# Optimization experiments

Hardware: AMD Instinct MI355X
Metric: run time of the kernel (lower is better)

## Reference

```python
import jax, jax.numpy as jnp
import numpy as np

INPUT_SIZE = 64
HIDDEN = 128
NUM_CLASSES = 4
BATCH = 512
SEQ = 1024


def setup_inputs() -> dict:
    key = jax.random.key(0)
    ks = jax.random.split(key, 11)
    s_in = 1.0 / np.sqrt(INPUT_SIZE)
    s_h = 1.0 / np.sqrt(HIDDEN)
    inp = {
        "x": jax.random.normal(ks[0], (BATCH, SEQ, INPUT_SIZE), dtype=jnp.float32),
        # layer1: x_proj (4H, in), h_proj (4H, H), each with bias
        "Wx1": jax.random.uniform(ks[1], (4 * HIDDEN, INPUT_SIZE), minval=-s_in, maxval=s_in),
        "bx1": jax.random.uniform(ks[2], (4 * HIDDEN,), minval=-s_in, maxval=s_in),
        "Wh1": jax.random.uniform(ks[3], (4 * HIDDEN, HIDDEN), minval=-s_h, maxval=s_h),
        "bh1": jax.random.uniform(ks[4], (4 * HIDDEN,), minval=-s_h, maxval=s_h),
        # layer2: x_proj (4H, H), h_proj (4H, H)
        "Wx2": jax.random.uniform(ks[5], (4 * HIDDEN, HIDDEN), minval=-s_h, maxval=s_h),
        "bx2": jax.random.uniform(ks[6], (4 * HIDDEN,), minval=-s_h, maxval=s_h),
        "Wh2": jax.random.uniform(ks[7], (4 * HIDDEN, HIDDEN), minval=-s_h, maxval=s_h),
        "bh2": jax.random.uniform(ks[8], (4 * HIDDEN,), minval=-s_h, maxval=s_h),
        # classifier head (num_classes, H)
        "Wc": jax.random.uniform(ks[9], (NUM_CLASSES, HIDDEN), minval=-s_h, maxval=s_h),
        "bc": jax.random.uniform(ks[10], (NUM_CLASSES,), minval=-s_h, maxval=s_h),
    }
    return inp


def _cell(gates, c_prev):
    # torch Linear gate order after chunk(4): i, f, g, o
    i, f, g, o = jnp.split(gates, 4, axis=-1)
    c = jax.nn.sigmoid(f) * c_prev + jax.nn.sigmoid(i) * jnp.tanh(g)
    h = jax.nn.sigmoid(o) * jnp.tanh(c)
    return h, c


def reference(x, Wx1, bx1, Wh1, bh1, Wx2, bx2, Wh2, bh2, Wc, bc):
    B = x.shape[0]
    H = Wh1.shape[1]
    # Precompute input projections for all timesteps in one big GEMM: (B,S,4H)
    xg1 = jnp.einsum("bsi,gi->bsg", x, Wx1) + bx1 + bh1  # fold both biases
    xg1_t = jnp.swapaxes(xg1, 0, 1)  # (S, B, 4H) for scan

    def step(carry, xg_t):
        h1, c1, h2, c2 = carry
        gates1 = xg_t + h1 @ Wh1.T
        h1, c1 = _cell(gates1, c1)
        gates2 = h1 @ Wx2.T + bx2 + h2 @ Wh2.T + bh2
        h2, c2 = _cell(gates2, c2)
        return (h1, c1, h2, c2), None

    z = jnp.zeros((B, H), dtype=x.dtype)
    (h1, c1, h2, c2), _ = jax.lax.scan(step, (z, z, z, z), xg1_t)
    logits = h2 @ Wc.T + bc  # (B, num_classes)
    return logits
```

## Files before the change

kernel.cpp:

```cpp
#include <hip/hip_runtime.h>
#include <hip/hip_fp16.h>

namespace {

constexpr int kS = 1024;
constexpr int kI = 64;
constexpr int kH = 128;

typedef _Float16 f16x8 __attribute__((ext_vector_type(8)));
typedef float    f32x4 __attribute__((ext_vector_type(4)));

#define MFMA16(a, b, c) __builtin_amdgcn_mfma_f32_16x16x32_f16((a), (b), (c), 0, 0, 0)

__device__ __forceinline__ float rcpf(float x) {
#if __has_builtin(__builtin_amdgcn_rcpf)
  return __builtin_amdgcn_rcpf(x);
#else
  return 1.0f / x;
#endif
}
__device__ __forceinline__ float sigf(float x)  { return rcpf(1.0f + __expf(-x)); }
__device__ __forceinline__ float tanhff(float x){ return 1.0f - 2.0f * rcpf(1.0f + __expf(2.0f * x)); }

__device__ __forceinline__ f16x8 afrag(const float* __restrict__ W, int row,
                                       int k0, int ld) {
  const float4* p = reinterpret_cast<const float4*>(W + (size_t)row * ld + k0);
  const float4 u = p[0], v = p[1];
  f16x8 a;
  a[0] = (_Float16)u.x; a[1] = (_Float16)u.y; a[2] = (_Float16)u.z; a[3] = (_Float16)u.w;
  a[4] = (_Float16)v.x; a[5] = (_Float16)v.y; a[6] = (_Float16)v.z; a[7] = (_Float16)v.w;
  return a;
}

__global__ __launch_bounds__(1024) void lstm_l1(
    const float* __restrict__ x, const float* __restrict__ Wx1,
    const float* __restrict__ bx1, const float* __restrict__ Wh1,
    const float* __restrict__ bh1, _Float16* __restrict__ h1out)
{
  const int tid  = threadIdx.x;
  const int b0   = blockIdx.x * 2;
  const int w    = tid >> 6;
  const int q    = (tid >> 4) & 3;
  const int n    = tid & 15;
  const bool real = (n < 2);

  __shared__ __align__(16) _Float16 xB[8][8][2][8];
  __shared__ __align__(16) _Float16 hB[2][16][2][8];
  __shared__ __align__(16) float    zslot[4];
  __shared__ float gbuf[2][512];

  f16x8 A[2][6];
  {
    const int rb = w * 32 + (tid & 15);
#pragma unroll
    for (int s = 0; s < 2; ++s) {
      const int row = rb + s * 16;
      A[s][0] = afrag(Wx1, row, q * 8,       kI);
      A[s][1] = afrag(Wx1, row, 32 + q * 8,  kI);
#pragma unroll
      for (int kt = 0; kt < 4; ++kt)
        A[s][2 + kt] = afrag(Wh1, row, kt * 32 + q * 8, kH);
    }
  }

  float bI = 0.f, bF = 0.f, bG = 0.f, bO = 0.f, cst = 0.f;
  if (tid < 256) {
    const int j = tid & 127;
    bI = bx1[j]       + bh1[j];
    bF = bx1[j + 128] + bh1[j + 128];
    bG = bx1[j + 256] + bh1[j + 256];
    bO = bx1[j + 384] + bh1[j + 384];
  }
  if (tid < 256)      reinterpret_cast<_Float16*>(hB)[tid] = (_Float16)0.f;
  else if (tid < 260) zslot[tid - 256] = 0.f;

  const int   off = q * 32 + n * 16;
  const char* zp  = reinterpret_cast<const char*>(zslot);

  for (int t0 = 0; t0 < kS; t0 += 8) {
    {
      const int st = tid >> 7, sn = (tid >> 6) & 1, sk = tid & 63;
      const float v = x[((size_t)(b0 + sn) * kS + (size_t)(t0 + st)) * kI + sk];
      xB[st][sk >> 3][sn][sk & 7] = (_Float16)v;
    }
    __syncthreads();

    for (int dt = 0; dt < 8; ++dt) {
      const int t = t0 + dt;
      const char* xb = reinterpret_cast<const char*>(&xB[dt][0][0][0]);
      const char* hb = reinterpret_cast<const char*>(&hB[t & 1][0][0][0]);
      const f16x8 bf0 = *reinterpret_cast<const f16x8*>(real ? xb + off       : zp);
      const f16x8 bf1 = *reinterpret_cast<const f16x8*>(real ? xb + 128 + off : zp);
      const f16x8 bf2 = *reinterpret_cast<const f16x8*>(real ? hb + off       : zp);
      const f16x8 bf3 = *reinterpret_cast<const f16x8*>(real ? hb + 128 + off : zp);
      const f16x8 bf4 = *reinterpret_cast<const f16x8*>(real ? hb + 256 + off : zp);
      const f16x8 bf5 = *reinterpret_cast<const f16x8*>(real ? hb + 384 + off : zp);

      f32x4 d0 = {0.f, 0.f, 0.f, 0.f}, d1 = {0.f, 0.f, 0.f, 0.f};
      d0 = MFMA16(A[0][0], bf0, d0);  d1 = MFMA16(A[1][0], bf0, d1);
      d0 = MFMA16(A[0][1], bf1, d0);  d1 = MFMA16(A[1][1], bf1, d1);
      d0 = MFMA16(A[0][2], bf2, d0);  d1 = MFMA16(A[1][2], bf2, d1);
      d0 = MFMA16(A[0][3], bf3, d0);  d1 = MFMA16(A[1][3], bf3, d1);
      d0 = MFMA16(A[0][4], bf4, d0);  d1 = MFMA16(A[1][4], bf4, d1);
      d0 = MFMA16(A[0][5], bf5, d0);  d1 = MFMA16(A[1][5], bf5, d1);

      if (real) {
        *reinterpret_cast<f32x4*>(&gbuf[n][w * 32 + q * 4])      = d0;
        *reinterpret_cast<f32x4*>(&gbuf[n][w * 32 + 16 + q * 4]) = d1;
      }
      __syncthreads();

      if (tid < 256) {
        const int cc = tid >> 7, j = tid & 127;
        const float gi = gbuf[cc][j]       + bI;
        const float gf = gbuf[cc][j + 128] + bF;
        const float gg = gbuf[cc][j + 256] + bG;
        const float go = gbuf[cc][j + 384] + bO;
        cst = sigf(gf) * cst + sigf(gi) * tanhff(gg);
        const float h = sigf(go) * tanhff(cst);
        hB[(t + 1) & 1][j >> 3][cc][j & 7] = (_Float16)h;
        h1out[((size_t)(b0 + cc) * kS + (size_t)t) * kH + j] = (_Float16)h;
      }
      __syncthreads();
    }
  }
}

__global__ __launch_bounds__(1024) void lstm_l2(
    const _Float16* __restrict__ h1in,
    const float* __restrict__ Wx2, const float* __restrict__ bx2,
    const float* __restrict__ Wh2, const float* __restrict__ bh2,
    const float* __restrict__ Wc,  const float* __restrict__ bc,
    float* __restrict__ out)
{
  const int tid  = threadIdx.x;
  const int b0   = blockIdx.x * 2;
  const int w    = tid >> 6;
  const int q    = (tid >> 4) & 3;
  const int n    = tid & 15;
  const bool real = (n < 2);

  __shared__ __align__(16) _Float16 h1B[8][16][2][8];
  __shared__ __align__(16) _Float16 h2B[2][16][2][8];
  __shared__ __align__(16) float    zslot[4];
  __shared__ float gbuf[2][512];
  __shared__ float hfin[2][128];

  f16x8 A[2][8];
  {
    const int rb = w * 32 + (tid & 15);
#pragma unroll
    for (int s = 0; s < 2; ++s) {
      const int row = rb + s * 16;
#pragma unroll
      for (int kt = 0; kt < 4; ++kt) {
        A[s][kt]     = afrag(Wx2, row, kt * 32 + q * 8, kH);
        A[s][4 + kt] = afrag(Wh2, row, kt * 32 + q * 8, kH);
      }
    }
  }

  float bI = 0.f, bF = 0.f, bG = 0.f, bO = 0.f, cst = 0.f;
  if (tid < 256) {
    const int j = tid & 127;
    bI = bx2[j]       + bh2[j];
    bF = bx2[j + 128] + bh2[j + 128];
    bG = bx2[j + 256] + bh2[j + 256];
    bO = bx2[j + 384] + bh2[j + 384];
  }
  if (tid < 256)      reinterpret_cast<_Float16*>(h2B)[tid] = (_Float16)0.f;
  else if (tid < 260) zslot[tid - 256] = 0.f;

  const int   off = q * 32 + n * 16;
  const char* zp  = reinterpret_cast<const char*>(zslot);

  for (int t0 = 0; t0 < kS; t0 += 8) {
    {
#pragma unroll
      for (int e = tid; e < 2048; e += 1024) {
        const int st = e >> 8, sn = (e >> 7) & 1, sk = e & 127;
        h1B[st][sk >> 3][sn][sk & 7] =
            h1in[((size_t)(b0 + sn) * kS + (size_t)(t0 + st)) * kH + sk];
      }
    }
    __syncthreads();

    for (int dt = 0; dt < 8; ++dt) {
      const int t = t0 + dt;
      const char* xb = reinterpret_cast<const char*>(&h1B[dt][0][0][0]);
      const char* hb = reinterpret_cast<const char*>(&h2B[t & 1][0][0][0]);

      f32x4 d0 = {0.f, 0.f, 0.f, 0.f}, d1 = {0.f, 0.f, 0.f, 0.f};
      {
        const f16x8 bf0 = *reinterpret_cast<const f16x8*>(real ? xb + off       : zp);
        const f16x8 bf1 = *reinterpret_cast<const f16x8*>(real ? xb + 128 + off : zp);
        const f16x8 bf2 = *reinterpret_cast<const f16x8*>(real ? xb + 256 + off : zp);
        const f16x8 bf3 = *reinterpret_cast<const f16x8*>(real ? xb + 384 + off : zp);
        d0 = MFMA16(A[0][0], bf0, d0);  d1 = MFMA16(A[1][0], bf0, d1);
        d0 = MFMA16(A[0][1], bf1, d0);  d1 = MFMA16(A[1][1], bf1, d1);
        d0 = MFMA16(A[0][2], bf2, d0);  d1 = MFMA16(A[1][2], bf2, d1);
        d0 = MFMA16(A[0][3], bf3, d0);  d1 = MFMA16(A[1][3], bf3, d1);
      }
#if __has_builtin(__builtin_amdgcn_sched_barrier)
      __builtin_amdgcn_sched_barrier(0);
#endif
      {
        const f16x8 bf4 = *reinterpret_cast<const f16x8*>(real ? hb + off       : zp);
        const f16x8 bf5 = *reinterpret_cast<const f16x8*>(real ? hb + 128 + off : zp);
        const f16x8 bf6 = *reinterpret_cast<const f16x8*>(real ? hb + 256 + off : zp);
        const f16x8 bf7 = *reinterpret_cast<const f16x8*>(real ? hb + 384 + off : zp);
        d0 = MFMA16(A[0][4], bf4, d0);  d1 = MFMA16(A[1][4], bf4, d1);
        d0 = MFMA16(A[0][5], bf5, d0);  d1 = MFMA16(A[1][5], bf5, d1);
        d0 = MFMA16(A[0][6], bf6, d0);  d1 = MFMA16(A[1][6], bf6, d1);
        d0 = MFMA16(A[0][7], bf7, d0);  d1 = MFMA16(A[1][7], bf7, d1);
      }

      if (real) {
        *reinterpret_cast<f32x4*>(&gbuf[n][w * 32 + q * 4])      = d0;
        *reinterpret_cast<f32x4*>(&gbuf[n][w * 32 + 16 + q * 4]) = d1;
      }
      __syncthreads();

      if (tid < 256) {
        const int cc = tid >> 7, j = tid & 127;
        const float gi = gbuf[cc][j]       + bI;
        const float gf = gbuf[cc][j + 128] + bF;
        const float gg = gbuf[cc][j + 256] + bG;
        const float go = gbuf[cc][j + 384] + bO;
        cst = sigf(gf) * cst + sigf(gi) * tanhff(gg);
        const float h = sigf(go) * tanhff(cst);
        h2B[(t + 1) & 1][j >> 3][cc][j & 7] = (_Float16)h;
        if (t == kS - 1) hfin[cc][j] = h;
      }
      __syncthreads();
    }
  }

  if (tid < 8) {
    const int m = tid & 3, c = tid >> 2;
    const float* wr = Wc + (size_t)m * kH;
    float s0 = 0.f, s1 = 0.f, s2 = 0.f, s3 = 0.f;
#pragma unroll
    for (int j = 0; j < kH; j += 4) {
      s0 = fmaf(wr[j],     hfin[c][j],     s0);
      s1 = fmaf(wr[j + 1], hfin[c][j + 1], s1);
      s2 = fmaf(wr[j + 2], hfin[c][j + 2], s2);
      s3 = fmaf(wr[j + 3], hfin[c][j + 3], s3);
    }
    out[(size_t)(b0 + c) * 4 + m] = bc[m] + ((s0 + s1) + (s2 + s3));
  }
}

}

extern "C" void kernel_launch(void* const* d_in, const int* in_sizes, int n_in,
                              void* d_out, int out_size, void* d_ws, size_t ws_size,
                              hipStream_t stream) {
  const float* x   = (const float*)d_in[0];
  const float* Wx1 = (const float*)d_in[1];
  const float* bx1 = (const float*)d_in[2];
  const float* Wh1 = (const float*)d_in[3];
  const float* bh1 = (const float*)d_in[4];
  const float* Wx2 = (const float*)d_in[5];
  const float* bx2 = (const float*)d_in[6];
  const float* Wh2 = (const float*)d_in[7];
  const float* bh2 = (const float*)d_in[8];
  const float* Wc  = (const float*)d_in[9];
  const float* bc  = (const float*)d_in[10];

  _Float16* h1 = (_Float16*)d_ws;

  hipLaunchKernelGGL(lstm_l1, dim3(256), dim3(1024), 0, stream,
                     x, Wx1, bx1, Wh1, bh1, h1);
  hipLaunchKernelGGL(lstm_l2, dim3(256), dim3(1024), 0, stream,
                     h1, Wx2, bx2, Wh2, bh2, Wc, bc, (float*)d_out);
}
```

Measured before the change: 1.858 ms.

## Process one batch element per block and raise MFMA wave priority

Each workgroup now handles a single sequence instead of two, which doubles the grid so more independent recurrences run concurrently across CUs. The MFMA B-operand layout is simplified so only one column is real and the zero-slot indirection is removed. The MFMA sections are wrapped in s_setprio to favour the latency-critical matrix work. This relies on two 1024-thread blocks co-residing per CU; otherwise the doubled grid would serialize.

```diff
diff --git a/kernel.cpp b/kernel.cpp
--- a/kernel.cpp
+++ b/kernel.cpp
@@ -21,6 +21,13 @@
 }
 __device__ __forceinline__ float sigf(float x)  { return rcpf(1.0f + __expf(-x)); }
 __device__ __forceinline__ float tanhff(float x){ return 1.0f - 2.0f * rcpf(1.0f + __expf(2.0f * x)); }
+
+template <int P>
+__device__ __forceinline__ void prio() {
+#if __has_builtin(__builtin_amdgcn_s_setprio)
+  __builtin_amdgcn_s_setprio(P);
+#endif
+}
 
 __device__ __forceinline__ f16x8 afrag(const float* __restrict__ W, int row,
                                        int k0, int ld) {
@@ -37,17 +44,16 @@
     const float* __restrict__ bx1, const float* __restrict__ Wh1,
     const float* __restrict__ bh1, _Float16* __restrict__ h1out)
 {
-  const int tid  = threadIdx.x;
-  const int b0   = blockIdx.x * 2;
-  const int w    = tid >> 6;
-  const int q    = (tid >> 4) & 3;
-  const int n    = tid & 15;
-  const bool real = (n < 2);
-
-  __shared__ __align__(16) _Float16 xB[8][8][2][8];
-  __shared__ __align__(16) _Float16 hB[2][16][2][8];
-  __shared__ __align__(16) float    zslot[4];
-  __shared__ float gbuf[2][512];
+  const int tid = threadIdx.x;
+  const int b   = blockIdx.x;
+  const int w   = tid >> 6;
+  const int q   = (tid >> 4) & 3;
+  const int n   = tid & 15;
+  const bool real = (n == 0);
+
+  __shared__ __align__(16) _Float16 xB[8][8][8];
+  __shared__ __align__(16) _Float16 hB[2][16][8];
+  __shared__ float gbuf[512];
 
   f16x8 A[2][6];
   {
@@ -55,8 +61,8 @@
 #pragma unroll
     for (int s = 0; s < 2; ++s) {
       const int row = rb + s * 16;
-      A[s][0] = afrag(Wx1, row, q * 8,       kI);
-      A[s][1] = afrag(Wx1, row, 32 + q * 8,  kI);
+      A[s][0] = afrag(Wx1, row, q * 8,      kI);
+      A[s][1] = afrag(Wx1, row, 32 + q * 8, kI);
 #pragma unroll
       for (int kt = 0; kt < 4; ++kt)
         A[s][2 + kt] = afrag(Wh1, row, kt * 32 + q * 8, kH);
@@ -64,62 +70,60 @@
   }
 
   float bI = 0.f, bF = 0.f, bG = 0.f, bO = 0.f, cst = 0.f;
-  if (tid < 256) {
-    const int j = tid & 127;
-    bI = bx1[j]       + bh1[j];
-    bF = bx1[j + 128] + bh1[j + 128];
-    bG = bx1[j + 256] + bh1[j + 256];
-    bO = bx1[j + 384] + bh1[j + 384];
-  }
-  if (tid < 256)      reinterpret_cast<_Float16*>(hB)[tid] = (_Float16)0.f;
-  else if (tid < 260) zslot[tid - 256] = 0.f;
-
-  const int   off = q * 32 + n * 16;
-  const char* zp  = reinterpret_cast<const char*>(zslot);
+  if (tid < 128) {
+    bI = bx1[tid]       + bh1[tid];
+    bF = bx1[tid + 128] + bh1[tid + 128];
+    bG = bx1[tid + 256] + bh1[tid + 256];
+    bO = bx1[tid + 384] + bh1[tid + 384];
+    reinterpret_cast<_Float16*>(hB)[tid] = (_Float16)0.f;
+  }
+
+  const int boff = real ? (q * 16) : 0;
 
   for (int t0 = 0; t0 < kS; t0 += 8) {
-    {
-      const int st = tid >> 7, sn = (tid >> 6) & 1, sk = tid & 63;
-      const float v = x[((size_t)(b0 + sn) * kS + (size_t)(t0 + st)) * kI + sk];
-      xB[st][sk >> 3][sn][sk & 7] = (_Float16)v;
+    if (tid < 512) {
+      const int st = tid >> 6, sk = tid & 63;
+      xB[st][sk >> 3][sk & 7] =
+          (_Float16)x[((size_t)b * kS + (size_t)(t0 + st)) * kI + sk];
     }
     __syncthreads();
 
     for (int dt = 0; dt < 8; ++dt) {
       const int t = t0 + dt;
-      const char* xb = reinterpret_cast<const char*>(&xB[dt][0][0][0]);
-      const char* hb = reinterpret_cast<const char*>(&hB[t & 1][0][0][0]);
-      const f16x8 bf0 = *reinterpret_cast<const f16x8*>(real ? xb + off       : zp);
-      const f16x8 bf1 = *reinterpret_cast<const f16x8*>(real ? xb + 128 + off : zp);
-      const f16x8 bf2 = *reinterpret_cast<const f16x8*>(real ? hb + off       : zp);
-      const f16x8 bf3 = *reinterpret_cast<const f16x8*>(real ? hb + 128 + off : zp);
-      const f16x8 bf4 = *reinterpret_cast<const f16x8*>(real ? hb + 256 + off : zp);
-      const f16x8 bf5 = *reinterpret_cast<const f16x8*>(real ? hb + 384 + off : zp);
+      const char* xb = reinterpret_cast<const char*>(&xB[dt][0][0]);
+      const char* hb = reinterpret_cast<const char*>(&hB[t & 1][0][0]);
+      const f16x8 bf0 = *reinterpret_cast<const f16x8*>(xb + boff);
+      const f16x8 bf1 = *reinterpret_cast<const f16x8*>(xb + 64  + boff);
+      const f16x8 bf2 = *reinterpret_cast<const f16x8*>(hb + boff);
+      const f16x8 bf3 = *reinterpret_cast<const f16x8*>(hb + 64  + boff);
+      const f16x8 bf4 = *reinterpret_cast<const f16x8*>(hb + 128 + boff);
+      const f16x8 bf5 = *reinterpret_cast<const f16x8*>(hb + 192 + boff);
 
       f32x4 d0 = {0.f, 0.f, 0.f, 0.f}, d1 = {0.f, 0.f, 0.f, 0.f};
+      prio<1>();
       d0 = MFMA16(A[0][0], bf0, d0);  d1 = MFMA16(A[1][0], bf0, d1);
       d0 = MFMA16(A[0][1], bf1, d0);  d1 = MFMA16(A[1][1], bf1, d1);
       d0 = MFMA16(A[0][2], bf2, d0);  d1 = MFMA16(A[1][2], bf2, d1);
       d0 = MFMA16(A[0][3], bf3, d0);  d1 = MFMA16(A[1][3], bf3, d1);
       d0 = MFMA16(A[0][4], bf4, d0);  d1 = MFMA16(A[1][4], bf4, d1);
       d0 = MFMA16(A[0][5], bf5, d0);  d1 = MFMA16(A[1][5], bf5, d1);
+      prio<0>();
 
       if (real) {
-        *reinterpret_cast<f32x4*>(&gbuf[n][w * 32 + q * 4])      = d0;
-        *reinterpret_cast<f32x4*>(&gbuf[n][w * 32 + 16 + q * 4]) = d1;
-      }
-      __syncthreads();
-
-      if (tid < 256) {
-        const int cc = tid >> 7, j = tid & 127;
-        const float gi = gbuf[cc][j]       + bI;
-        const float gf = gbuf[cc][j + 128] + bF;
-        const float gg = gbuf[cc][j + 256] + bG;
-        const float go = gbuf[cc][j + 384] + bO;
+        *reinterpret_cast<f32x4*>(&gbuf[w * 32 + q * 4])      = d0;
+        *reinterpret_cast<f32x4*>(&gbuf[w * 32 + 16 + q * 4]) = d1;
+      }
+      __syncthreads();
+
+      if (tid < 128) {
+        const float gi = gbuf[tid]       + bI;
+        const float gf = gbuf[tid + 128] + bF;
+        const float gg = gbuf[tid + 256] + bG;
+        const float go = gbuf[tid + 384] + bO;
         cst = sigf(gf) * cst + sigf(gi) * tanhff(gg);
         const float h = sigf(go) * tanhff(cst);
-        hB[(t + 1) & 1][j >> 3][cc][j & 7] = (_Float16)h;
-        h1out[((size_t)(b0 + cc) * kS + (size_t)t) * kH + j] = (_Float16)h;
+        hB[(t + 1) & 1][tid >> 3][tid & 7] = (_Float16)h;
+        h1out[((size_t)b * kS + (size_t)t) * kH + tid] = (_Float16)h;
       }
       __syncthreads();
     }
@@ -133,18 +137,17 @@
     const float* __restrict__ Wc,  const float* __restrict__ bc,
     float* __restrict__ out)
 {
-  const int tid  = threadIdx.x;
-  const int b0   = blockIdx.x * 2;
-  const int w    = tid >> 6;
-  const int q    = (tid >> 4) & 3;
-  const int n    = tid & 15;
-  const bool real = (n < 2);
-
-  __shared__ __align__(16) _Float16 h1B[8][16][2][8];
-  __shared__ __align__(16) _Float16 h2B[2][16][2][8];
-  __shared__ __align__(16) float    zslot[4];
-  __shared__ float gbuf[2][512];
-  __shared__ float hfin[2][128];
+  const int tid = threadIdx.x;
+  const int b   = blockIdx.x;
+  const int w   = tid >> 6;
+  const int q   = (tid >> 4) & 3;
+  const int n   = tid & 15;
+  const bool real = (n == 0);
+
+  __shared__ __align__(16) _Float16 h1B[8][16][8];
+  __shared__ __align__(16) _Float16 h2B[2][16][8];
+  __shared__ float gbuf[512];
+  __shared__ float hfin[128];
 
   f16x8 A[2][8];
   {
@@ -161,93 +164,89 @@
   }
 
   float bI = 0.f, bF = 0.f, bG = 0.f, bO = 0.f, cst = 0.f;
-  if (tid < 256) {
-    const int j = tid & 127;
-    bI = bx2[j]       + bh2[j];
-    bF = bx2[j + 128] + bh2[j + 128];
-    bG = bx2[j + 256] + bh2[j + 256];
-    bO = bx2[j + 384] + bh2[j + 384];
-  }
-  if (tid < 256)      reinterpret_cast<_Float16*>(h2B)[tid] = (_Float16)0.f;
-  else if (tid < 260) zslot[tid - 256] = 0.f;
-
-  const int   off = q * 32 + n * 16;
-  const char* zp  = reinterpret_cast<const char*>(zslot);
+  if (tid < 128) {
+    bI = bx2[tid]       + bh2[tid];
+    bF = bx2[tid + 128] + bh2[tid + 128];
+    bG = bx2[tid + 256] + bh2[tid + 256];
+    bO = bx2[tid + 384] + bh2[tid + 384];
+    reinterpret_cast<_Float16*>(h2B)[tid] = (_Float16)0.f;
+  }
+
+  const int boff = real ? (q * 16) : 0;
 
   for (int t0 = 0; t0 < kS; t0 += 8) {
     {
-#pragma unroll
-      for (int e = tid; e < 2048; e += 1024) {
-        const int st = e >> 8, sn = (e >> 7) & 1, sk = e & 127;
-        h1B[st][sk >> 3][sn][sk & 7] =
-            h1in[((size_t)(b0 + sn) * kS + (size_t)(t0 + st)) * kH + sk];
-      }
+      const int st = tid >> 7, sk = tid & 127;
+      h1B[st][sk >> 3][sk & 7] =
+          h1in[((size_t)b * kS + (size_t)(t0 + st)) * kH + sk];
     }
     __syncthreads();
 
     for (int dt = 0; dt < 8; ++dt) {
       const int t = t0 + dt;
-      const char* xb = reinterpret_cast<const char*>(&h1B[dt][0][0][0]);
-      const char* hb = reinterpret_cast<const char*>(&h2B[t & 1][0][0][0]);
+      const char* xb = reinterpret_cast<const char*>(&h1B[dt][0][0]);
+      const char* hb = reinterpret_cast<const char*>(&h2B[t & 1][0][0]);
 
       f32x4 d0 = {0.f, 0.f, 0.f, 0.f}, d1 = {0.f, 0.f, 0.f, 0.f};
       {
-        const f16x8 bf0 = *reinterpret_cast<const f16x8*>(real ? xb + off       : zp);
-        const f16x8 bf1 = *reinterpret_cast<const f16x8*>(real ? xb + 128 + off : zp);
-        const f16x8 bf2 = *reinterpret_cast<const f16x8*>(real ? xb + 256 + off : zp);
-        const f16x8 bf3 = *reinterpret_cast<const f16x8*>(real ? xb + 384 + off : zp);
+        const f16x8 bf0 = *reinterpret_cast<const f16x8*>(xb + boff);
+        const f16x8 bf1 = *reinterpret_cast<const f16x8*>(xb + 64  + boff);
+        const f16x8 bf2 = *reinterpret_cast<const f16x8*>(xb + 128 + boff);
+        const f16x8 bf3 = *reinterpret_cast<const f16x8*>(xb + 192 + boff);
+        prio<1>();
         d0 = MFMA16(A[0][0], bf0, d0);  d1 = MFMA16(A[1][0], bf0, d1);
         d0 = MFMA16(A[0][1], bf1, d0);  d1 = MFMA16(A[1][1], bf1, d1);
         d0 = MFMA16(A[0][2], bf2, d0);  d1 = MFMA16(A[1][2], bf2, d1);
         d0 = MFMA16(A[0][3], bf3, d0);  d1 = MFMA16(A[1][3], bf3, d1);
+        prio<0>();
       }
 #if __has_builtin(__builtin_amdgcn_sched_barrier)
       __builtin_amdgcn_sched_barrier(0);
 #endif
       {
-        const f16x8 bf4 = *reinterpret_cast<const f16x8*>(real ? hb + off       : zp);
-        const f16x8 bf5 = *reinterpret_cast<const f16x8*>(real ? hb + 128 + off : zp);
-        const f16x8 bf6 = *reinterpret_cast<const f16x8*>(real ? hb + 256 + off : zp);
-        const f16x8 bf7 = *reinterpret_cast<const f16x8*>(real ? hb + 384 + off : zp);
+        const f16x8 bf4 = *reinterpret_cast<const f16x8*>(hb + boff);
+        const f16x8 bf5 = *reinterpret_cast<const f16x8*>(hb + 64  + boff);
+        const f16x8 bf6 = *reinterpret_cast<const f16x8*>(hb + 128 + boff);
+        const f16x8 bf7 = *reinterpret_cast<const f16x8*>(hb + 192 + boff);
+        prio<1>();
         d0 = MFMA16(A[0][4], bf4, d0);  d1 = MFMA16(A[1][4], bf4, d1);
         d0 = MFMA16(A[0][5], bf5, d0);  d1 = MFMA16(A[1][5], bf5, d1);
         d0 = MFMA16(A[0][6], bf6, d0);  d1 = MFMA16(A[1][6], bf6, d1);
         d0 = MFMA16(A[0][7], bf7, d0);  d1 = MFMA16(A[1][7], bf7, d1);
+        prio<0>();
       }
 
       if (real) {
-        *reinterpret_cast<f32x4*>(&gbuf[n][w * 32 + q * 4])      = d0;
-        *reinterpret_cast<f32x4*>(&gbuf[n][w * 32 + 16 + q * 4]) = d1;
-      }
-      __syncthreads();
-
-      if (tid < 256) {
-        const int cc = tid >> 7, j = tid & 127;
-        const float gi = gbuf[cc][j]       + bI;
-        const float gf = gbuf[cc][j + 128] + bF;
-        const float gg = gbuf[cc][j + 256] + bG;
-        const float go = gbuf[cc][j + 384] + bO;
+        *reinterpret_cast<f32x4*>(&gbuf[w * 32 + q * 4])      = d0;
+        *reinterpret_cast<f32x4*>(&gbuf[w * 32 + 16 + q * 4]) = d1;
+      }
+      __syncthreads();
+
+      if (tid < 128) {
+        const float gi = gbuf[tid]       + bI;
+        const float gf = gbuf[tid + 128] + bF;
+        const float gg = gbuf[tid + 256] + bG;
+        const float go = gbuf[tid + 384] + bO;
         cst = sigf(gf) * cst + sigf(gi) * tanhff(gg);
         const float h = sigf(go) * tanhff(cst);
-        h2B[(t + 1) & 1][j >> 3][cc][j & 7] = (_Float16)h;
-        if (t == kS - 1) hfin[cc][j] = h;
-      }
-      __syncthreads();
-    }
-  }
-
-  if (tid < 8) {
-    const int m = tid & 3, c = tid >> 2;
-    const float* wr = Wc + (size_t)m * kH;
+        h2B[(t + 1) & 1][tid >> 3][tid & 7] = (_Float16)h;
+        if (t == kS - 1) hfin[tid] = h;
+      }
+      __syncthreads();
+    }
+  }
+
+  if (tid < 4) {
+    const float* wr = Wc + (size_t)tid * kH;
     float s0 = 0.f, s1 = 0.f, s2 = 0.f, s3 = 0.f;
 #pragma unroll
     for (int j = 0; j < kH; j += 4) {
-      s0 = fmaf(wr[j],     hfin[c][j],     s0);
-      s1 = fmaf(wr[j + 1], hfin[c][j + 1], s1);
-      s2 = fmaf(wr[j + 2], hfin[c][j + 2], s2);
-      s3 = fmaf(wr[j + 3], hfin[c][j + 3], s3);
-    }
-    out[(size_t)(b0 + c) * 4 + m] = bc[m] + ((s0 + s1) + (s2 + s3));
+      s0 = fmaf(wr[j],     hfin[j],     s0);
+      s1 = fmaf(wr[j + 1], hfin[j + 1], s1);
+      s2 = fmaf(wr[j + 2], hfin[j + 2], s2);
+      s3 = fmaf(wr[j + 3], hfin[j + 3], s3);
+    }
+    out[(size_t)b * 4 + tid] = bc[tid] + ((s0 + s1) + (s2 + s3));
   }
 }
 
@@ -270,8 +269,8 @@
 
   _Float16* h1 = (_Float16*)d_ws;
 
-  hipLaunchKernelGGL(lstm_l1, dim3(256), dim3(1024), 0, stream,
+  hipLaunchKernelGGL(lstm_l1, dim3(512), dim3(1024), 0, stream,
                      x, Wx1, bx1, Wh1, bh1, h1);
-  hipLaunchKernelGGL(lstm_l2, dim3(256), dim3(1024), 0, stream,
+  hipLaunchKernelGGL(lstm_l2, dim3(512), dim3(1024), 0, stream,
                      h1, Wx2, bx2, Wh2, bh2, Wc, bc, (float*)d_out);
 }
```

Result: slower. 3.092 ms (+66.4%).

## Batch input projections per 8-step chunk and shrink per-step recurrent MFMA work

Applied to the files above, without the earlier changes.

Hoists the input-projection MFMAs out of the per-timestep loop. They are now computed once per 8-step chunk, with all 16 (timestep,batch) columns filling the MFMA N dimension, and stored in an xg shared buffer. The per-step critical path then only runs the recurrent Wh matmul (4 MFMA pairs instead of 6 or 8), using a new h layout with clamped column selection instead of zero-slot loads. It also adds s_setprio around the recurrent MFMAs and packs x loads into half2 stores. The cost is an extra sync per chunk and a large padded shared-memory buffer.

```diff
diff --git a/kernel.cpp b/kernel.cpp
--- a/kernel.cpp
+++ b/kernel.cpp
@@ -21,6 +21,20 @@
 }
 __device__ __forceinline__ float sigf(float x)  { return rcpf(1.0f + __expf(-x)); }
 __device__ __forceinline__ float tanhff(float x){ return 1.0f - 2.0f * rcpf(1.0f + __expf(2.0f * x)); }
+
+template <int P>
+__device__ __forceinline__ void prio() {
+#if __has_builtin(__builtin_amdgcn_s_setprio)
+  __builtin_amdgcn_s_setprio(P);
+#endif
+}
+
+__device__ __forceinline__ unsigned packf2(float lo, float hi) {
+  _Float16 a = (_Float16)lo, b = (_Float16)hi;
+  unsigned short ua = __builtin_bit_cast(unsigned short, a);
+  unsigned short ub = __builtin_bit_cast(unsigned short, b);
+  return (unsigned)ua | ((unsigned)ub << 16);
+}
 
 __device__ __forceinline__ f16x8 afrag(const float* __restrict__ W, int row,
                                        int k0, int ld) {
@@ -40,26 +54,25 @@
   const int tid  = threadIdx.x;
   const int b0   = blockIdx.x * 2;
   const int w    = tid >> 6;
-  const int q    = (tid >> 4) & 3;
-  const int n    = tid & 15;
-  const bool real = (n < 2);
-
-  __shared__ __align__(16) _Float16 xB[8][8][2][8];
-  __shared__ __align__(16) _Float16 hB[2][16][2][8];
-  __shared__ __align__(16) float    zslot[4];
+  const int lane = tid & 63;
+  const int q    = lane >> 4;
+  const int n    = lane & 15;
+
+  __shared__ __align__(16) _Float16 xF[8][16][8];
+  __shared__ __align__(16) _Float16 h1B[2][2][16][8];
+  __shared__ float xg[512][17];
   __shared__ float gbuf[2][512];
 
-  f16x8 A[2][6];
+  f16x8 Ax[2][2], Ah[2][4];
   {
-    const int rb = w * 32 + (tid & 15);
+    const int rb = w * 32 + n;
 #pragma unroll
     for (int s = 0; s < 2; ++s) {
       const int row = rb + s * 16;
-      A[s][0] = afrag(Wx1, row, q * 8,       kI);
-      A[s][1] = afrag(Wx1, row, 32 + q * 8,  kI);
-#pragma unroll
-      for (int kt = 0; kt < 4; ++kt)
-        A[s][2 + kt] = afrag(Wh1, row, kt * 32 + q * 8, kH);
+#pragma unroll
+      for (int kt = 0; kt < 2; ++kt) Ax[s][kt] = afrag(Wx1, row, kt * 32 + q * 8, kI);
+#pragma unroll
+      for (int kt = 0; kt < 4; ++kt) Ah[s][kt] = afrag(Wh1, row, kt * 32 + q * 8, kH);
     }
   }
 
@@ -70,56 +83,72 @@
     bF = bx1[j + 128] + bh1[j + 128];
     bG = bx1[j + 256] + bh1[j + 256];
     bO = bx1[j + 384] + bh1[j + 384];
-  }
-  if (tid < 256)      reinterpret_cast<_Float16*>(hB)[tid] = (_Float16)0.f;
-  else if (tid < 260) zslot[tid - 256] = 0.f;
-
-  const int   off = q * 32 + n * 16;
-  const char* zp  = reinterpret_cast<const char*>(zslot);
+    reinterpret_cast<_Float16*>(&h1B[1][0][0][0])[tid] = (_Float16)0.f;
+  }
+
+  const int csel  = (n < 2) ? n : 0;
+  const char* h1base = reinterpret_cast<const char*>(&h1B[0][0][0][0]);
 
   for (int t0 = 0; t0 < kS; t0 += 8) {
+    if (tid < 512) {
+      const int col = tid >> 5, sk2 = tid & 31;
+      const int c = col & 1, dt = col >> 1;
+      const float2 v = *reinterpret_cast<const float2*>(
+          x + ((size_t)(b0 + c) * kS + (size_t)(t0 + dt)) * kI + sk2 * 2);
+      const int k = sk2 * 2;
+      *reinterpret_cast<unsigned*>(&xF[k >> 3][col][k & 7]) = packf2(v.x, v.y);
+    }
+    __syncthreads();
+
     {
-      const int st = tid >> 7, sn = (tid >> 6) & 1, sk = tid & 63;
-      const float v = x[((size_t)(b0 + sn) * kS + (size_t)(t0 + st)) * kI + sk];
-      xB[st][sk >> 3][sn][sk & 7] = (_Float16)v;
+      const char* xb = reinterpret_cast<const char*>(&xF[0][0][0]);
+      f32x4 e0 = {0.f, 0.f, 0.f, 0.f}, e1 = {0.f, 0.f, 0.f, 0.f};
+#pragma unroll
+      for (int kt = 0; kt < 2; ++kt) {
+        const f16x8 bf = *reinterpret_cast<const f16x8*>(
+            xb + (((kt * 4 + q) * 16 + n) << 4));
+        e0 = MFMA16(Ax[0][kt], bf, e0);
+        e1 = MFMA16(Ax[1][kt], bf, e1);
+      }
+#pragma unroll
+      for (int r = 0; r < 4; ++r) {
+        xg[w * 32 + q * 4 + r][n]      = e0[r];
+        xg[w * 32 + 16 + q * 4 + r][n] = e1[r];
+      }
     }
     __syncthreads();
 
     for (int dt = 0; dt < 8; ++dt) {
       const int t = t0 + dt;
-      const char* xb = reinterpret_cast<const char*>(&xB[dt][0][0][0]);
-      const char* hb = reinterpret_cast<const char*>(&hB[t & 1][0][0][0]);
-      const f16x8 bf0 = *reinterpret_cast<const f16x8*>(real ? xb + off       : zp);
-      const f16x8 bf1 = *reinterpret_cast<const f16x8*>(real ? xb + 128 + off : zp);
-      const f16x8 bf2 = *reinterpret_cast<const f16x8*>(real ? hb + off       : zp);
-      const f16x8 bf3 = *reinterpret_cast<const f16x8*>(real ? hb + 128 + off : zp);
-      const f16x8 bf4 = *reinterpret_cast<const f16x8*>(real ? hb + 256 + off : zp);
-      const f16x8 bf5 = *reinterpret_cast<const f16x8*>(real ? hb + 384 + off : zp);
+      const int rp = (t + 1) & 1;
+      const char* hb = h1base + ((rp * 2 + csel) << 8);
 
       f32x4 d0 = {0.f, 0.f, 0.f, 0.f}, d1 = {0.f, 0.f, 0.f, 0.f};
-      d0 = MFMA16(A[0][0], bf0, d0);  d1 = MFMA16(A[1][0], bf0, d1);
-      d0 = MFMA16(A[0][1], bf1, d0);  d1 = MFMA16(A[1][1], bf1, d1);
-      d0 = MFMA16(A[0][2], bf2, d0);  d1 = MFMA16(A[1][2], bf2, d1);
-      d0 = MFMA16(A[0][3], bf3, d0);  d1 = MFMA16(A[1][3], bf3, d1);
-      d0 = MFMA16(A[0][4], bf4, d0);  d1 = MFMA16(A[1][4], bf4, d1);
-      d0 = MFMA16(A[0][5], bf5, d0);  d1 = MFMA16(A[1][5], bf5, d1);
-
-      if (real) {
+      prio<1>();
+#pragma unroll
+      for (int kt = 0; kt < 4; ++kt) {
+        const f16x8 bf = *reinterpret_cast<const f16x8*>(hb + ((kt * 4 + q) << 4));
+        d0 = MFMA16(Ah[0][kt], bf, d0);
+        d1 = MFMA16(Ah[1][kt], bf, d1);
+      }
+      prio<0>();
+
+      if (n < 2) {
         *reinterpret_cast<f32x4*>(&gbuf[n][w * 32 + q * 4])      = d0;
         *reinterpret_cast<f32x4*>(&gbuf[n][w * 32 + 16 + q * 4]) = d1;
       }
       __syncthreads();
 
       if (tid < 256) {
-        const int cc = tid >> 7, j = tid & 127;
-        const float gi = gbuf[cc][j]       + bI;
-        const float gf = gbuf[cc][j + 128] + bF;
-        const float gg = gbuf[cc][j + 256] + bG;
-        const float go = gbuf[cc][j + 384] + bO;
+        const int c = tid >> 7, j = tid & 127, col = dt * 2 + c;
+        const float gi = xg[j][col]       + gbuf[c][j]       + bI;
+        const float gf = xg[j + 128][col] + gbuf[c][j + 128] + bF;
+        const float gg = xg[j + 256][col] + gbuf[c][j + 256] + bG;
+        const float go = xg[j + 384][col] + gbuf[c][j + 384] + bO;
         cst = sigf(gf) * cst + sigf(gi) * tanhff(gg);
         const float h = sigf(go) * tanhff(cst);
-        hB[(t + 1) & 1][j >> 3][cc][j & 7] = (_Float16)h;
-        h1out[((size_t)(b0 + cc) * kS + (size_t)t) * kH + j] = (_Float16)h;
+        h1B[t & 1][c][j >> 3][j & 7] = (_Float16)h;
+        h1out[((size_t)(b0 + c) * kS + (size_t)t) * kH + j] = (_Float16)h;
       }
       __syncthreads();
     }
@@ -136,26 +165,26 @@
   const int tid  = threadIdx.x;
   const int b0   = blockIdx.x * 2;
   const int w    = tid >> 6;
-  const int q    = (tid >> 4) & 3;
-  const int n    = tid & 15;
-  const bool real = (n < 2);
-
-  __shared__ __align__(16) _Float16 h1B[8][16][2][8];
-  __shared__ __align__(16) _Float16 h2B[2][16][2][8];
-  __shared__ __align__(16) float    zslot[4];
+  const int lane = tid & 63;
+  const int q    = lane >> 4;
+  const int n    = lane & 15;
+
+  __shared__ __align__(16) _Float16 h1F[16][16][8];
+  __shared__ __align__(16) _Float16 h2B[2][2][16][8];
+  __shared__ float xg[512][17];
   __shared__ float gbuf[2][512];
   __shared__ float hfin[2][128];
 
-  f16x8 A[2][8];
+  f16x8 Ax[2][4], Ah[2][4];
   {
-    const int rb = w * 32 + (tid & 15);
+    const int rb = w * 32 + n;
 #pragma unroll
     for (int s = 0; s < 2; ++s) {
       const int row = rb + s * 16;
 #pragma unroll
       for (int kt = 0; kt < 4; ++kt) {
-        A[s][kt]     = afrag(Wx2, row, kt * 32 + q * 8, kH);
-        A[s][4 + kt] = afrag(Wh2, row, kt * 32 + q * 8, kH);
+        Ax[s][kt] = afrag(Wx2, row, kt * 32 + q * 8, kH);
+        Ah[s][kt] = afrag(Wh2, row, kt * 32 + q * 8, kH);
       }
     }
   }
@@ -167,70 +196,72 @@
     bF = bx2[j + 128] + bh2[j + 128];
     bG = bx2[j + 256] + bh2[j + 256];
     bO = bx2[j + 384] + bh2[j + 384];
-  }
-  if (tid < 256)      reinterpret_cast<_Float16*>(h2B)[tid] = (_Float16)0.f;
-  else if (tid < 260) zslot[tid - 256] = 0.f;
-
-  const int   off = q * 32 + n * 16;
-  const char* zp  = reinterpret_cast<const char*>(zslot);
+    reinterpret_cast<_Float16*>(&h2B[1][0][0][0])[tid] = (_Float16)0.f;
+  }
+
+  const int csel = (n < 2) ? n : 0;
+  const char* h2base = reinterpret_cast<const char*>(&h2B[0][0][0][0]);
 
   for (int t0 = 0; t0 < kS; t0 += 8) {
     {
-#pragma unroll
-      for (int e = tid; e < 2048; e += 1024) {
-        const int st = e >> 8, sn = (e >> 7) & 1, sk = e & 127;
-        h1B[st][sk >> 3][sn][sk & 7] =
-            h1in[((size_t)(b0 + sn) * kS + (size_t)(t0 + st)) * kH + sk];
+      const int col = tid >> 6, sk2 = tid & 63;
+      const int c = col & 1, dt = col >> 1;
+      const unsigned v = *reinterpret_cast<const unsigned*>(
+          h1in + ((size_t)(b0 + c) * kS + (size_t)(t0 + dt)) * kH + sk2 * 2);
+      const int k = sk2 * 2;
+      *reinterpret_cast<unsigned*>(&h1F[k >> 3][col][k & 7]) = v;
+    }
+    __syncthreads();
+
+    {
+      const char* xb = reinterpret_cast<const char*>(&h1F[0][0][0]);
+      f32x4 e0 = {0.f, 0.f, 0.f, 0.f}, e1 = {0.f, 0.f, 0.f, 0.f};
+#pragma unroll
+      for (int kt = 0; kt < 4; ++kt) {
+        const f16x8 bf = *reinterpret_cast<const f16x8*>(
+            xb + (((kt * 4 + q) * 16 + n) << 4));
+        e0 = MFMA16(Ax[0][kt], bf, e0);
+        e1 = MFMA16(Ax[1][kt], bf, e1);
+      }
+#pragma unroll
+      for (int r = 0; r < 4; ++r) {
+        xg[w * 32 + q * 4 + r][n]      = e0[r];
+        xg[w * 32 + 16 + q * 4 + r][n] = e1[r];
       }
     }
     __syncthreads();
 
     for (int dt = 0; dt < 8; ++dt) {
       const int t = t0 + dt;
-      const char* xb = reinterpret_cast<const char*>(&h1B[dt][0][0][0]);
-      const char* hb = reinterpret_cast<const char*>(&h2B[t & 1][0][0][0]);
+      const int rp = (t + 1) & 1;
+      const char* hb = h2base + ((rp * 2 + csel) << 8);
 
       f32x4 d0 = {0.f, 0.f, 0.f, 0.f}, d1 = {0.f, 0.f, 0.f, 0.f};
-      {
-        const f16x8 bf0 = *reinterpret_cast<const f16x8*>(real ? xb + off       : zp);
-        const f16x8 bf1 = *reinterpret_cast<const f16x8*>(real ? xb + 128 + off : zp);
-        const f16x8 bf2 = *reinterpret_cast<const f16x8*>(real ? xb + 256 + off : zp);
-        const f16x8 bf3 = *reinterpret_cast<const f16x8*>(real ? xb + 384 + off : zp);
-        d0 = MFMA16(A[0][0], bf0, d0);  d1 = MFMA16(A[1][0], bf0, d1);
-        d0 = MFMA16(A[0][1], bf1, d0);  d1 = MFMA16(A[1][1], bf1, d1);
-        d0 = MFMA16(A[0][2], bf2, d0);  d1 = MFMA16(A[1][2], bf2, d1);
-        d0 = MFMA16(A[0][3], bf3, d0);  d1 = MFMA16(A[1][3], bf3, d1);
-      }
-#if __has_builtin(__builtin_amdgcn_sched_barrier)
-      __builtin_amdgcn_sched_barrier(0);
-#endif
-      {
-        const f16x8 bf4 = *reinterpret_cast<const f16x8*>(real ? hb + off       : zp);
-        const f16x8 bf5 = *reinterpret_cast<const f16x8*>(real ? hb + 128 + off : zp);
-        const f16x8 bf6 = *reinterpret_cast<const f16x8*>(real ? hb + 256 + off : zp);
-        const f16x8 bf7 = *reinterpret_cast<const f16x8*>(real ? hb + 384 + off : zp);
-        d0 = MFMA16(A[0][4], bf4, d0);  d1 = MFMA16(A[1][4], bf4, d1);
-        d0 = MFMA16(A[0][5], bf5, d0);  d1 = MFMA16(A[1][5], bf5, d1);
-        d0 = MFMA16(A[0][6], bf6, d0);  d1 = MFMA16(A[1][6], bf6, d1);
-        d0 = MFMA16(A[0][7], bf7, d0);  d1 = MFMA16(A[1][7], bf7, d1);
-      }
-
-      if (real) {
+      prio<1>();
+#pragma unroll
+      for (int kt = 0; kt < 4; ++kt) {
+        const f16x8 bf = *reinterpret_cast<const f16x8*>(hb + ((kt * 4 + q) << 4));
+        d0 = MFMA16(Ah[0][kt], bf, d0);
+        d1 = MFMA16(Ah[1][kt], bf, d1);
+      }
+      prio<0>();
+
+      if (n < 2) {
         *reinterpret_cast<f32x4*>(&gbuf[n][w * 32 + q * 4])      = d0;
         *reinterpret_cast<f32x4*>(&gbuf[n][w * 32 + 16 + q * 4]) = d1;
       }
       __syncthreads();
 
       if (tid < 256) {
-        const int cc = tid >> 7, j = tid & 127;
-        const float gi = gbuf[cc][j]       + bI;
-        const float gf = gbuf[cc][j + 128] + bF;
-        const float gg = gbuf[cc][j + 256] + bG;
-        const float go = gbuf[cc][j + 384] + bO;
+        const int c = tid >> 7, j = tid & 127, col = dt * 2 + c;
+        const float gi = xg[j][col]       + gbuf[c][j]       + bI;
+        const float gf = xg[j + 128][col] + gbuf[c][j + 128] + bF;
+        const float gg = xg[j + 256][col] + gbuf[c][j + 256] + bG;
+        const float go = xg[j + 384][col] + gbuf[c][j + 384] + bO;
         cst = sigf(gf) * cst + sigf(gi) * tanhff(gg);
         const float h = sigf(go) * tanhff(cst);
-        h2B[(t + 1) & 1][j >> 3][cc][j & 7] = (_Float16)h;
-        if (t == kS - 1) hfin[cc][j] = h;
+        h2B[t & 1][c][j >> 3][j & 7] = (_Float16)h;
+        if (t == kS - 1) hfin[c][j] = h;
       }
       __syncthreads();
     }
```

New measurement: 1.537 ms. -17.3%, faster.
